# Optimization experiments

Hardware: AMD Instinct MI355X
Metric: run time of the kernel (lower is better)

The kernel has to match this reference:

```python
import jax, jax.numpy as jnp
import numpy as np

IN_DIM = 4096
OUT_DIM = 4096
RANK = 16
BATCH = 4
SEQ = 2048


def setup_inputs() -> dict:
    key = jax.random.key(0)
    ks = jax.random.split(key, 7)
    x = jax.random.normal(ks[0], (BATCH, SEQ, IN_DIM), dtype=jnp.float32)
    org_weight = jax.random.normal(ks[1], (OUT_DIM, IN_DIM), dtype=jnp.float32) * 0.02
    org_bias = jax.random.normal(ks[2], (OUT_DIM,), dtype=jnp.float32) * 0.02
    hada_w1_a = jax.random.normal(ks[3], (OUT_DIM, RANK), dtype=jnp.float32) * 0.1
    hada_w1_b = jax.random.normal(ks[4], (RANK, IN_DIM), dtype=jnp.float32)
    hada_w2_a = jax.random.normal(ks[5], (OUT_DIM, RANK), dtype=jnp.float32) * 0.1
    hada_w2_b = jax.random.normal(ks[6], (RANK, IN_DIM), dtype=jnp.float32)
    scalar = jnp.ones((), dtype=jnp.float32)
    return {
        "x": x,
        "org_weight": org_weight,
        "org_bias": org_bias,
        "hada_w1_a": hada_w1_a,
        "hada_w1_b": hada_w1_b,
        "hada_w2_a": hada_w2_a,
        "hada_w2_b": hada_w2_b,
        "scalar": scalar,
    }


def reference(x, org_weight, org_bias, hada_w1_a, hada_w1_b, hada_w2_a, hada_w2_b, scalar):
    scale = jnp.asarray(1.0, dtype=hada_w1_b.dtype)   # self.scale = 1.0
    multiplier = jnp.asarray(1.0, dtype=x.dtype)       # self.multiplier = 1.0
    # base = F.linear(x, org_weight, org_bias)
    base = jnp.einsum("bsi,oi->bso", x, org_weight) + org_bias
    # diff_weight = (w1a @ w1b) * (w2a @ w2b) * scale * scalar  -> [out, in]
    diff_weight = (hada_w1_a @ hada_w1_b) * (hada_w2_a @ hada_w2_b) * scale * scalar
    # delta = F.linear(x, diff_weight * multiplier)
    delta = jnp.einsum("bsi,oi->bso", x, diff_weight * multiplier)
    return base + delta
```

## Files before the change

kernel.cpp:

```cpp
#include <hip/hip_runtime.h>

#define IN_DIM 4096
#define OUT_DIM 4096
#define RANK 16
#define MDIM 8192

typedef unsigned short ushort_t;
typedef __attribute__((ext_vector_type(8))) short short8;
typedef __attribute__((ext_vector_type(4))) float floatx4;
typedef __attribute__((ext_vector_type(4))) ushort_t ushort4_t;

__device__ __forceinline__ ushort_t f2b(float f) {
    union { float f; unsigned int i; } v; v.f = f;
    unsigned int u = v.i;
    u += 0x7FFFu + ((u >> 16) & 1u);
    return (ushort_t)(u >> 16);
}

#define GLOAD_LDS16(gp, lp)                                                    \
    __builtin_amdgcn_global_load_lds(                                          \
        (__attribute__((address_space(1))) void*)(gp),                         \
        (__attribute__((address_space(3))) void*)(lp), 16, 0, 0)

__global__ __launch_bounds__(256) void convx_kernel(
    const float4* __restrict__ x, ushort4_t* __restrict__ xb, int n4)
{
    int i = blockIdx.x * blockDim.x + threadIdx.x;
    int stride = gridDim.x * blockDim.x;
    for (; i < n4; i += stride) {
        float4 v = x[i];
        ushort4_t o;
        o.x = f2b(v.x); o.y = f2b(v.y); o.z = f2b(v.z); o.w = f2b(v.w);
        xb[i] = o;
    }
}

__global__ __launch_bounds__(256) void weff_kernel(
    const float* __restrict__ orgw,
    const float* __restrict__ w1a, const float* __restrict__ w1b,
    const float* __restrict__ w2a, const float* __restrict__ w2b,
    const float* __restrict__ scalar,
    ushort_t* __restrict__ weff)
{
    __shared__ float s1b[RANK][256];
    __shared__ float s2b[RANK][256];
    __shared__ float s1a[64 * RANK];
    __shared__ float s2a[64 * RANK];

    const int t  = threadIdx.x;
    const int i0 = blockIdx.x * 256;
    const int o0 = blockIdx.y * 64;

    #pragma unroll
    for (int r = 0; r < RANK; ++r) {
        s1b[r][t] = w1b[r * IN_DIM + i0 + t];
        s2b[r][t] = w2b[r * IN_DIM + i0 + t];
    }
    for (int e = t; e < 64 * RANK; e += 256) {
        s1a[e] = w1a[o0 * RANK + e];
        s2a[e] = w2a[o0 * RANK + e];
    }
    __syncthreads();

    const float sc = scalar[0];
    for (int o = 0; o < 64; ++o) {
        float a1 = 0.f, a2 = 0.f;
        #pragma unroll
        for (int r = 0; r < RANK; ++r) {
            a1 += s1a[o * RANK + r] * s1b[r][t];
            a2 += s2a[o * RANK + r] * s2b[r][t];
        }
        const int idx = (o0 + o) * IN_DIM + i0 + t;
        weff[idx] = f2b(orgw[idx] + a1 * a2 * sc);
    }
}

#define BM 256
#define BN 256
#define BK 64

#define STAGE_A(buf, half, kcol)                                               \
    do {                                                                       \
        GLOAD_LDS16(gX0 + (size_t)(half) * (128 * IN_DIM) + (kcol),            \
                    (short*)&lA[buf][half][0][0] + w * 512);                   \
        GLOAD_LDS16(gX1 + (size_t)(half) * (128 * IN_DIM) + (kcol),            \
                    (short*)&lA[buf][half][0][0] + 4096 + w * 512);            \
    } while (0)

#define STAGE_B(buf, half, kcol)                                               \
    do {                                                                       \
        GLOAD_LDS16(gW0 + (size_t)(half) * (128 * IN_DIM) + (kcol),            \
                    (short*)&lB[buf][half][0][0] + w * 512);                   \
        GLOAD_LDS16(gW1 + (size_t)(half) * (128 * IN_DIM) + (kcol),            \
                    (short*)&lB[buf][half][0][0] + 4096 + w * 512);            \
    } while (0)

#define MFMA_(d, a, b) (d) = __builtin_amdgcn_mfma_f32_16x16x32_bf16((a), (b), (d), 0, 0, 0)

#define HALF_ITER(aB, bB, S1, S2, S3, S4)                                      \
    do {                                                                       \
        short8 a_lo[4][2], a_hi[4][2], b_lo[2][2], b_hi[2][2];                 \
                         \
        _Pragma("unroll")                                                      \
        for (int mi = 0; mi < 4; ++mi) {                                       \
            a_lo[mi][0] = *(const short8*)((aB) + mi * 1024 + ok0);            \
            a_lo[mi][1] = *(const short8*)((aB) + mi * 1024 + ok1);            \
        }                                                                      \
        _Pragma("unroll")                                                      \
        for (int ni = 0; ni < 2; ++ni) {                                       \
            b_lo[ni][0] = *(const short8*)((bB) + ni * 1024 + ok0);            \
            b_lo[ni][1] = *(const short8*)((bB) + ni * 1024 + ok1);            \
        }                                                                      \
        S1;                                                                    \
        __builtin_amdgcn_s_barrier();                                          \
        asm volatile("s_waitcnt lgkmcnt(0)" ::: "memory");                     \
        __builtin_amdgcn_s_setprio(1);                                         \
        _Pragma("unroll")                                                      \
        for (int mi = 0; mi < 4; ++mi)                                         \
            _Pragma("unroll")                                                  \
            for (int ni = 0; ni < 2; ++ni) {                                   \
                MFMA_(acc[mi][ni], a_lo[mi][0], b_lo[ni][0]);                  \
                MFMA_(acc[mi][ni], a_lo[mi][1], b_lo[ni][1]);                  \
            }                                                                  \
        __builtin_amdgcn_s_setprio(0);                                         \
        __builtin_amdgcn_s_barrier();                                          \
                                 \
        _Pragma("unroll")                                                      \
        for (int mi = 0; mi < 4; ++mi) {                                       \
            a_hi[mi][0] = *(const short8*)((aB) + 4096 + mi * 1024 + ok0);     \
            a_hi[mi][1] = *(const short8*)((aB) + 4096 + mi * 1024 + ok1);     \
        }                                                                      \
        S2;                                                                    \
        __builtin_amdgcn_s_barrier();                                          \
        asm volatile("s_waitcnt lgkmcnt(0)" ::: "memory");                     \
        __builtin_amdgcn_s_setprio(1);                                         \
        _Pragma("unroll")                                                      \
        for (int mi = 0; mi < 4; ++mi)                                         \
            _Pragma("unroll")                                                  \
            for (int ni = 0; ni < 2; ++ni) {                                   \
                MFMA_(acc[4 + mi][ni], a_hi[mi][0], b_lo[ni][0]);              \
                MFMA_(acc[4 + mi][ni], a_hi[mi][1], b_lo[ni][1]);              \
            }                                                                  \
        __builtin_amdgcn_s_setprio(0);                                         \
        __builtin_amdgcn_s_barrier();                                          \
                                 \
        _Pragma("unroll")                                                      \
        for (int ni = 0; ni < 2; ++ni) {                                       \
            b_hi[ni][0] = *(const short8*)((bB) + 2048 + ni * 1024 + ok0);     \
            b_hi[ni][1] = *(const short8*)((bB) + 2048 + ni * 1024 + ok1);     \
        }                                                                      \
        S3;                                                                    \
        __builtin_amdgcn_s_barrier();                                          \
        asm volatile("s_waitcnt lgkmcnt(0)" ::: "memory");                     \
        __builtin_amdgcn_s_setprio(1);                                         \
        _Pragma("unroll")                                                      \
        for (int mi = 0; mi < 4; ++mi)                                         \
            _Pragma("unroll")                                                  \
            for (int ni = 0; ni < 2; ++ni) {                                   \
                MFMA_(acc[4 + mi][2 + ni], a_hi[mi][0], b_hi[ni][0]);          \
                MFMA_(acc[4 + mi][2 + ni], a_hi[mi][1], b_hi[ni][1]);          \
            }                                                                  \
        __builtin_amdgcn_s_setprio(0);                                         \
        __builtin_amdgcn_s_barrier();                                          \
           \
        S4;                                                                    \
        __builtin_amdgcn_s_barrier();                                          \
        __builtin_amdgcn_s_setprio(1);                                         \
        _Pragma("unroll")                                                      \
        for (int mi = 0; mi < 4; ++mi)                                         \
            _Pragma("unroll")                                                  \
            for (int ni = 0; ni < 2; ++ni) {                                   \
                MFMA_(acc[mi][2 + ni], a_lo[mi][0], b_hi[ni][0]);              \
                MFMA_(acc[mi][2 + ni], a_lo[mi][1], b_hi[ni][1]);              \
            }                                                                  \
        __builtin_amdgcn_s_setprio(0);                                         \
        asm volatile("s_waitcnt vmcnt(4)" ::: "memory");                       \
        __builtin_amdgcn_s_barrier();                                          \
    } while (0)

__global__ __launch_bounds__(512, 2) void gemm_kernel(
    const ushort_t* __restrict__ X,
    const ushort_t* __restrict__ W,
    const float* __restrict__ bias,
    float* __restrict__ out)
{
    __shared__ __align__(16) short lA[2][2][128][64];
    __shared__ __align__(16) short lB[2][2][128][64];

    const int t    = threadIdx.x;
    const int w    = t >> 6;
    const int lane = t & 63;
    const int quad = lane >> 4;
    const int r16  = lane & 15;
    const int wm   = w >> 2;
    const int wn   = w & 3;

    const int bid = blockIdx.y * gridDim.x + blockIdx.x;
    const int swz = (bid & 7) * 64 + (bid >> 3);
    const int m0  = (swz >> 4) * BM;
    const int n0  = (swz & 15) * BN;

    const int s0  = w * 64 + lane;
    const int s1  = 512 + s0;
    const int r0  = s0 >> 3, r1 = s1 >> 3;
    const int k80 = (s0 & 7) ^ (r0 & 7);
    const int k81 = (s1 & 7) ^ (r1 & 7);
    const ushort_t* gX0 = X + (size_t)(m0 + r0) * IN_DIM + k80 * 8;
    const ushort_t* gX1 = X + (size_t)(m0 + r1) * IN_DIM + k81 * 8;
    const ushort_t* gW0 = W + (size_t)(n0 + r0) * IN_DIM + k80 * 8;
    const ushort_t* gW1 = W + (size_t)(n0 + r1) * IN_DIM + k81 * 8;

    const short* aB0 = &lA[0][wm][r16][0];
    const short* aB1 = &lA[1][wm][r16][0];
    const short* bB0 = &lB[0][wn >> 1][(wn & 1) * 64 + r16][0];
    const short* bB1 = &lB[1][wn >> 1][(wn & 1) * 64 + r16][0];
    const int ok0 = ((0 + quad) ^ (r16 & 7)) << 3;
    const int ok1 = ((4 + quad) ^ (r16 & 7)) << 3;

    floatx4 acc[8][4];
    #pragma unroll
    for (int i = 0; i < 8; ++i)
        #pragma unroll
        for (int j = 0; j < 4; ++j)
            acc[i][j] = (floatx4){0.f, 0.f, 0.f, 0.f};

    STAGE_A(0, 0, 0);
    STAGE_A(0, 1, 0);
    STAGE_B(0, 0, 0);
    STAGE_B(0, 1, 0);
    STAGE_A(1, 0, 64);
    STAGE_A(1, 1, 64);
    asm volatile("s_waitcnt vmcnt(4)" ::: "memory");
    __builtin_amdgcn_s_barrier();

    for (int it = 0; it < IN_DIM / 128; ++it) {
        const int kmax = IN_DIM - 64;
        int kB1 = it * 128 + 64;  if (kB1 > kmax) kB1 = kmax;
        int kA2 = it * 128 + 128; if (kA2 > kmax) kA2 = kmax;
        int kA3 = it * 128 + 192; if (kA3 > kmax) kA3 = kmax;

        HALF_ITER(aB0, bB0,
                  STAGE_B(1, 0, kB1), STAGE_B(1, 1, kB1),
                  STAGE_A(0, 0, kA2), STAGE_A(0, 1, kA2));
        HALF_ITER(aB1, bB1,
                  STAGE_B(0, 0, kA2), STAGE_B(0, 1, kA2),
                  STAGE_A(1, 0, kA3), STAGE_A(1, 1, kA3));
    }

    #pragma unroll
    for (int ni = 0; ni < 4; ++ni) {
        const int gn = n0 + wn * 64 + ni * 16 + r16;
        const float bv = bias[gn];
        #pragma unroll
        for (int mi = 0; mi < 8; ++mi) {
            const int gm = m0 + wm * 128 + mi * 16 + quad * 4;
            #pragma unroll
            for (int rr = 0; rr < 4; ++rr)
                out[(size_t)(gm + rr) * OUT_DIM + gn] = acc[mi][ni][rr] + bv;
        }
    }
}

extern "C" void kernel_launch(void* const* d_in, const int* in_sizes, int n_in,
                              void* d_out, int out_size, void* d_ws, size_t ws_size,
                              hipStream_t stream) {
    const float* x      = (const float*)d_in[0];
    const float* orgw   = (const float*)d_in[1];
    const float* bias   = (const float*)d_in[2];
    const float* w1a    = (const float*)d_in[3];
    const float* w1b    = (const float*)d_in[4];
    const float* w2a    = (const float*)d_in[5];
    const float* w2b    = (const float*)d_in[6];
    const float* scalar = (const float*)d_in[7];

    ushort_t* xb   = (ushort_t*)d_ws;
    ushort_t* weff = (ushort_t*)d_ws + (size_t)MDIM * IN_DIM;
    float* out = (float*)d_out;

    const int n4 = MDIM * IN_DIM / 4;
    convx_kernel<<<2048, 256, 0, stream>>>((const float4*)x, (ushort4_t*)xb, n4);
    weff_kernel<<<dim3(IN_DIM / 256, OUT_DIM / 64), 256, 0, stream>>>(
        orgw, w1a, w1b, w2a, w2b, scalar, weff);
    gemm_kernel<<<dim3(OUT_DIM / BN, MDIM / BM), 512, 0, stream>>>(
        xb, weff, bias, out);
}
```

Baseline: 598.4 us.

## Prefetch all LDS fragments early in GEMM half-iteration and vectorize weff kernel

```diff
diff --git a/kernel.cpp b/kernel.cpp
--- a/kernel.cpp
+++ b/kernel.cpp
@@ -9,6 +9,7 @@
 typedef __attribute__((ext_vector_type(8))) short short8;
 typedef __attribute__((ext_vector_type(4))) float floatx4;
 typedef __attribute__((ext_vector_type(4))) ushort_t ushort4_t;
+typedef __attribute__((ext_vector_type(2))) ushort_t ushort2_t;
 
 __device__ __forceinline__ ushort_t f2b(float f) {
     union { float f; unsigned int i; } v; v.f = f;
@@ -42,36 +43,56 @@
     const float* __restrict__ scalar,
     ushort_t* __restrict__ weff)
 {
-    __shared__ float s1b[RANK][256];
-    __shared__ float s2b[RANK][256];
     __shared__ float s1a[64 * RANK];
     __shared__ float s2a[64 * RANK];
 
     const int t  = threadIdx.x;
-    const int i0 = blockIdx.x * 256;
+    const int i0 = blockIdx.x * 512 + t * 2;
     const int o0 = blockIdx.y * 64;
 
-    #pragma unroll
-    for (int r = 0; r < RANK; ++r) {
-        s1b[r][t] = w1b[r * IN_DIM + i0 + t];
-        s2b[r][t] = w2b[r * IN_DIM + i0 + t];
-    }
     for (int e = t; e < 64 * RANK; e += 256) {
         s1a[e] = w1a[o0 * RANK + e];
         s2a[e] = w2a[o0 * RANK + e];
     }
+
+    float b1[RANK][2], b2[RANK][2];
+    #pragma unroll
+    for (int r = 0; r < RANK; ++r) {
+        const float2 v1 = *(const float2*)&w1b[r * IN_DIM + i0];
+        const float2 v2 = *(const float2*)&w2b[r * IN_DIM + i0];
+        b1[r][0] = v1.x; b1[r][1] = v1.y;
+        b2[r][0] = v2.x; b2[r][1] = v2.y;
+    }
     __syncthreads();
 
     const float sc = scalar[0];
     for (int o = 0; o < 64; ++o) {
-        float a1 = 0.f, a2 = 0.f;
+        float4 a1v[4], a2v[4];
         #pragma unroll
-        for (int r = 0; r < RANK; ++r) {
-            a1 += s1a[o * RANK + r] * s1b[r][t];
-            a2 += s2a[o * RANK + r] * s2b[r][t];
+        for (int j = 0; j < 4; ++j) {
+            a1v[j] = *(const float4*)&s1a[o * RANK + j * 4];
+            a2v[j] = *(const float4*)&s2a[o * RANK + j * 4];
         }
-        const int idx = (o0 + o) * IN_DIM + i0 + t;
-        weff[idx] = f2b(orgw[idx] + a1 * a2 * sc);
+        float p1_0 = 0.f, p1_1 = 0.f, p2_0 = 0.f, p2_1 = 0.f;
+        #pragma unroll
+        for (int j = 0; j < 4; ++j) {
+            #pragma unroll
+            for (int k = 0; k < 4; ++k) {
+                const int r = j * 4 + k;
+                const float a1 = (k == 0) ? a1v[j].x : (k == 1) ? a1v[j].y
+                               : (k == 2) ? a1v[j].z : a1v[j].w;
+                const float a2 = (k == 0) ? a2v[j].x : (k == 1) ? a2v[j].y
+                               : (k == 2) ? a2v[j].z : a2v[j].w;
+                p1_0 += a1 * b1[r][0]; p1_1 += a1 * b1[r][1];
+                p2_0 += a2 * b2[r][0]; p2_1 += a2 * b2[r][1];
+            }
+        }
+        const size_t idx = (size_t)(o0 + o) * IN_DIM + i0;
+        const float2 ov = *(const float2*)&orgw[idx];
+        ushort2_t st;
+        st.x = f2b(ov.x + p1_0 * p2_0 * sc);
+        st.y = f2b(ov.y + p1_1 * p2_1 * sc);
+        *(ushort2_t*)&weff[idx] = st;
     }
 }
 
@@ -100,7 +121,8 @@
 #define HALF_ITER(aB, bB, S1, S2, S3, S4)                                      \
     do {                                                                       \
         short8 a_lo[4][2], a_hi[4][2], b_lo[2][2], b_hi[2][2];                 \
-                         \
+        S1;                                                                    \
+                           \
         _Pragma("unroll")                                                      \
         for (int mi = 0; mi < 4; ++mi) {                                       \
             a_lo[mi][0] = *(const short8*)((aB) + mi * 1024 + ok0);            \
@@ -111,9 +133,24 @@
             b_lo[ni][0] = *(const short8*)((bB) + ni * 1024 + ok0);            \
             b_lo[ni][1] = *(const short8*)((bB) + ni * 1024 + ok1);            \
         }                                                                      \
-        S1;                                                                    \
-        __builtin_amdgcn_s_barrier();                                          \
-        asm volatile("s_waitcnt lgkmcnt(0)" ::: "memory");                     \
+        asm volatile("" ::: "memory");                  \
+                                     \
+        _Pragma("unroll")                                                      \
+        for (int mi = 0; mi < 4; ++mi) {                                       \
+            a_hi[mi][0] = *(const short8*)((aB) + 4096 + mi * 1024 + ok0);     \
+            a_hi[mi][1] = *(const short8*)((aB) + 4096 + mi * 1024 + ok1);     \
+        }                                                                      \
+        asm volatile("" ::: "memory");                  \
+                                     \
+        _Pragma("unroll")                                                      \
+        for (int ni = 0; ni < 2; ++ni) {                                       \
+            b_hi[ni][0] = *(const short8*)((bB) + 2048 + ni * 1024 + ok0);     \
+            b_hi[ni][1] = *(const short8*)((bB) + 2048 + ni * 1024 + ok1);     \
+        }                                                                      \
+          \
+        __builtin_amdgcn_s_barrier();                                          \
+        asm volatile("s_waitcnt lgkmcnt(12)" ::: "memory");                    \
+        __builtin_amdgcn_sched_barrier(0);                                     \
         __builtin_amdgcn_s_setprio(1);                                         \
         _Pragma("unroll")                                                      \
         for (int mi = 0; mi < 4; ++mi)                                         \
@@ -124,15 +161,11 @@
             }                                                                  \
         __builtin_amdgcn_s_setprio(0);                                         \
         __builtin_amdgcn_s_barrier();                                          \
-                                 \
-        _Pragma("unroll")                                                      \
-        for (int mi = 0; mi < 4; ++mi) {                                       \
-            a_hi[mi][0] = *(const short8*)((aB) + 4096 + mi * 1024 + ok0);     \
-            a_hi[mi][1] = *(const short8*)((aB) + 4096 + mi * 1024 + ok1);     \
-        }                                                                      \
+                         \
         S2;                                                                    \
         __builtin_amdgcn_s_barrier();                                          \
-        asm volatile("s_waitcnt lgkmcnt(0)" ::: "memory");                     \
+        asm volatile("s_waitcnt lgkmcnt(4)" ::: "memory");                     \
+        __builtin_amdgcn_sched_barrier(0);                                     \
         __builtin_amdgcn_s_setprio(1);                                         \
         _Pragma("unroll")                                                      \
         for (int mi = 0; mi < 4; ++mi)                                         \
@@ -143,15 +176,11 @@
             }                                                                  \
         __builtin_amdgcn_s_setprio(0);                                         \
         __builtin_amdgcn_s_barrier();                                          \
-                                 \
-        _Pragma("unroll")                                                      \
-        for (int ni = 0; ni < 2; ++ni) {                                       \
-            b_hi[ni][0] = *(const short8*)((bB) + 2048 + ni * 1024 + ok0);     \
-            b_hi[ni][1] = *(const short8*)((bB) + 2048 + ni * 1024 + ok1);     \
-        }                                                                      \
+                                     \
         S3;                                                                    \
         __builtin_amdgcn_s_barrier();                                          \
         asm volatile("s_waitcnt lgkmcnt(0)" ::: "memory");                     \
+        __builtin_amdgcn_sched_barrier(0);                                     \
         __builtin_amdgcn_s_setprio(1);                                         \
         _Pragma("unroll")                                                      \
         for (int mi = 0; mi < 4; ++mi)                                         \
@@ -162,7 +191,7 @@
             }                                                                  \
         __builtin_amdgcn_s_setprio(0);                                         \
         __builtin_amdgcn_s_barrier();                                          \
-           \
+                  \
         S4;                                                                    \
         __builtin_amdgcn_s_barrier();                                          \
         __builtin_amdgcn_s_setprio(1);                                         \
@@ -279,7 +308,7 @@
 
     const int n4 = MDIM * IN_DIM / 4;
     convx_kernel<<<2048, 256, 0, stream>>>((const float4*)x, (ushort4_t*)xb, n4);
-    weff_kernel<<<dim3(IN_DIM / 256, OUT_DIM / 64), 256, 0, stream>>>(
+    weff_kernel<<<dim3(IN_DIM / 512, OUT_DIM / 64), 256, 0, stream>>>(
         orgw, w1a, w1b, w2a, w2b, scalar, weff);
     gemm_kernel<<<dim3(OUT_DIM / BN, MDIM / BM), 512, 0, stream>>>(
         xb, weff, bias, out);
```

Measured after the change: 630.0 us. +5.3%, slower.
